# Performance work log

Hardware: AMD Instinct MI355X
Metric: run time of the kernel (lower is better)

Reference implementation:

```python
import jax, jax.numpy as jnp
import numpy as np
import math

G, NPG, D = 64, 2048, 128   # graphs, nodes per graph, feature dim
DEG = 16
N = G * NPG
E = N * DEG
VOCAB = 100000
RATIO = 0.8


def setup_inputs() -> dict:
    key = jax.random.key(0)
    ks = jax.random.split(key, 24)
    node_ids = jax.random.randint(ks[0], (N, 1), 0, VOCAB)
    # within-graph edges: endpoints in [0, NPG) per graph, then add graph offset
    within = jax.random.randint(ks[1], (2, G, NPG * DEG), 0, NPG)
    offs = (jnp.arange(G) * NPG)[None, :, None]
    edge_index = (within + offs).reshape(2, E)
    batch = jnp.repeat(jnp.arange(G), NPG)
    f = lambda k, shape: jax.random.normal(k, shape, dtype=jnp.float32) * 0.05
    return dict(
        node_ids=node_ids, edge_index=edge_index, batch=batch,
        emb=f(ks[2], (VOCAB, D)),
        Wl1=f(ks[3], (D, D)), Wr1=f(ks[4], (D, D)), bl1=f(ks[5], (D,)), pw1=f(ks[6], (D,)),
        Wl2=f(ks[7], (D, D)), Wr2=f(ks[8], (D, D)), bl2=f(ks[9], (D,)), pw2=f(ks[10], (D,)),
        Wl3=f(ks[11], (D, D)), Wr3=f(ks[12], (D, D)), bl3=f(ks[13], (D,)), pw3=f(ks[14], (D,)),
        W1=f(ks[15], (128, 256)), b1=f(ks[16], (128,)),
        W2=f(ks[17], (64, 128)), b2=f(ks[18], (64,)),
        W3=f(ks[19], (1, 64)), b3=f(ks[20], (1,)),
    )


def sage(x, src, dst, emask, Wl, bl, Wr):
    # PyG SAGEConv (mean aggr): lin_l(mean_j x_j) + lin_r(x_i); lin_r has no bias
    n = x.shape[0]
    msg = x[src] * emask[:, None].astype(x.dtype)
    dstm = jnp.where(emask, dst, n)  # dummy segment for invalid edges
    s = jax.ops.segment_sum(msg, dstm, num_segments=n + 1)[:n]
    c = jax.ops.segment_sum(emask.astype(x.dtype), dstm, num_segments=n + 1)[:n]
    mean = s / jnp.maximum(c, 1.0)[:, None]
    return mean @ Wl.T + bl + x @ Wr.T


def topk_pool(x, src, dst, emask, w, n_per):
    # PyG TopKPooling: score = tanh(x.w/||w||), keep top ceil(ratio*n) per graph,
    # scale kept features by score, remap/filter edges.
    n = x.shape[0]
    g = n // n_per
    k = math.ceil(RATIO * n_per)
    score = jnp.tanh((x @ w) / jnp.linalg.norm(w))
    ts, ti = jax.lax.top_k(score.reshape(g, n_per), k)  # [g, k]
    perm = (ti + (jnp.arange(g) * n_per)[:, None]).reshape(-1)  # old global idx
    x_new = x[perm] * ts.reshape(-1)[:, None]
    n_new = g * k
    new_of_old = jnp.full((n,), n_new, dtype=jnp.int32).at[perm].set(
        jnp.arange(n_new, dtype=jnp.int32))
    sn, dn = new_of_old[src], new_of_old[dst]
    em = emask & (sn < n_new) & (dn < n_new)
    sn = jnp.where(em, sn, 0)
    dn = jnp.where(em, dn, n_new)
    return x_new, sn, dn, em, k


def readout(x, k):
    # cat([global_max_pool, global_mean_pool]) with equal-size graphs
    g = x.shape[0] // k
    xr = x.reshape(g, k, -1)
    return jnp.concatenate([xr.max(axis=1), xr.mean(axis=1)], axis=1)


def reference(node_ids, edge_index, batch, emb,
              Wl1, Wr1, bl1, pw1, Wl2, Wr2, bl2, pw2, Wl3, Wr3, bl3, pw3,
              W1, b1, W2, b2, W3, b3):
    x = emb[node_ids.squeeze(1)]                       # [N, 128]
    src, dst = edge_index[0], edge_index[1]
    em = jnp.ones((src.shape[0],), dtype=bool)

    x = jax.nn.relu(sage(x, src, dst, em, Wl1, bl1, Wr1))
    x, src, dst, em, k1 = topk_pool(x, src, dst, em, pw1, NPG)
    x1 = readout(x, k1)

    x = jax.nn.relu(sage(x, src, dst, em, Wl2, bl2, Wr2))
    x, src, dst, em, k2 = topk_pool(x, src, dst, em, pw2, k1)
    x2 = readout(x, k2)

    x = jax.nn.relu(sage(x, src, dst, em, Wl3, bl3, Wr3))
    x, src, dst, em, k3 = topk_pool(x, src, dst, em, pw3, k2)
    x3 = readout(x, k3)

    h = x1 + x2 + x3                                   # [G, 256]
    h = jax.nn.relu(h @ W1.T + b1)
    h = jax.nn.relu(h @ W2.T + b2)                     # dropout = identity (eval)
    return jax.nn.sigmoid(h @ W3.T + b3).squeeze(1)    # [G]
```

## Files before the change

### kernel.cpp

```cpp
#include <hip/hip_runtime.h>
#include <hip/hip_bf16.h>
#include <float.h>

typedef _Float16 f16x8 __attribute__((ext_vector_type(8)));
typedef float f32x4 __attribute__((ext_vector_type(4)));

#define GRAPHS 64
#define NPG 2048
#define DIM 128
#define NNODES (GRAPHS * NPG)
#define NEDGES (NNODES * 16)
#define ECAP 32768
#define NSB 8
#define RSL 8
#define RPB 256

__global__ __launch_bounds__(256) void embed_kernel(const int* __restrict__ ids,
    const float* __restrict__ emb, _Float16* __restrict__ xh) {
  int idx = blockIdx.x * 256 + threadIdx.x;
  int nd = idx >> 4, part = idx & 15;
  int id = ids[nd];
  const float* src = emb + (size_t)id * 128 + part * 8;
  float4 a = *(const float4*)(src);
  float4 b = *(const float4*)(src + 4);
  f16x8 o;
  o[0] = (_Float16)a.x; o[1] = (_Float16)a.y; o[2] = (_Float16)a.z; o[3] = (_Float16)a.w;
  o[4] = (_Float16)b.x; o[5] = (_Float16)b.y; o[6] = (_Float16)b.z; o[7] = (_Float16)b.w;
  *(f16x8*)(xh + (size_t)nd * 128 + part * 8) = o;
}

__global__ __launch_bounds__(256) void convert_w(const float* __restrict__ Wl,
    const float* __restrict__ Wr, _Float16* __restrict__ wh) {
  int qq = blockIdx.x * 256 + threadIdx.x;
  int ks = qq >> 9, nf = (qq >> 6) & 7, l = qq & 63;
  int ncol = nf * 16 + (l & 15);
  int k0 = (ks & 3) * 32 + ((l >> 4) << 3);
  const float* wsrc = ((ks < 4) ? Wl : Wr) + ncol * 128 + k0;
  float4 a = *(const float4*)wsrc;
  float4 b = *(const float4*)(wsrc + 4);
  f16x8 w;
  w[0] = (_Float16)a.x; w[1] = (_Float16)a.y; w[2] = (_Float16)a.z; w[3] = (_Float16)a.w;
  w[4] = (_Float16)b.x; w[5] = (_Float16)b.y; w[6] = (_Float16)b.z; w[7] = (_Float16)b.w;
  *(f16x8*)(wh + (size_t)qq * 8) = w;
}

__global__ __launch_bounds__(1024) void csr_hist(const int* __restrict__ src,
    const int* __restrict__ dst, int np, int* __restrict__ part) {
  __shared__ int hist[2048];
  int x = blockIdx.x;
  int s = x & 7, q = x >> 3;
  int b = q & (NSB - 1), gh = q >> 3;
  int g = gh * 8 + s;
  int tid = threadIdx.x;
  for (int i = tid; i < 2048; i += 1024) hist[i] = 0;
  __syncthreads();
  int e0 = g * ECAP + b * (ECAP / NSB);
  int nodebase = g * np;
  for (int e = tid; e < ECAP / NSB; e += 1024) {
    atomicAdd(&hist[dst[e0 + e] - nodebase], 1);
  }
  __syncthreads();
  for (int i = tid; i < np; i += 1024) part[((size_t)(g * NSB + b)) * 2048 + i] = hist[i];
}

__global__ __launch_bounds__(1024) void csr_scan(const int* __restrict__ part, int np,
    int* __restrict__ offb, int* __restrict__ deg, int* __restrict__ curs) {
  __shared__ int psum[1024];
  int g = blockIdx.x, tid = threadIdx.x;
  int i0 = 2 * tid, i1 = 2 * tid + 1;
  int p0[NSB], p1[NSB];
  int c0 = 0, c1 = 0;
#pragma unroll
  for (int b = 0; b < NSB; ++b) {
    p0[b] = (i0 < np) ? part[((size_t)(g * NSB + b)) * 2048 + i0] : 0;
    p1[b] = (i1 < np) ? part[((size_t)(g * NSB + b)) * 2048 + i1] : 0;
    c0 += p0[b]; c1 += p1[b];
  }
  int pair = c0 + c1;
  psum[tid] = pair;
  for (int s = 1; s < 1024; s <<= 1) {
    __syncthreads();
    int t = (tid >= s) ? psum[tid - s] : 0;
    __syncthreads();
    psum[tid] += t;
  }
  int excl = psum[tid] - pair;
  int ebase = g * ECAP;
  int nodebase = g * np;
  if (i0 < np) {
    int off = ebase + excl;
    offb[nodebase + i0] = off;
    deg[nodebase + i0] = c0;
    int cur = off;
#pragma unroll
    for (int b = 0; b < NSB; ++b) { curs[((size_t)(g * NSB + b)) * 2048 + i0] = cur; cur += p0[b]; }
  }
  if (i1 < np) {
    int off = ebase + excl + c0;
    offb[nodebase + i1] = off;
    deg[nodebase + i1] = c1;
    int cur = off;
#pragma unroll
    for (int b = 0; b < NSB; ++b) { curs[((size_t)(g * NSB + b)) * 2048 + i1] = cur; cur += p1[b]; }
  }
}

__global__ __launch_bounds__(1024) void csr_place(const int* __restrict__ src,
    const int* __restrict__ dst, int np, const int* __restrict__ curs,
    int* __restrict__ esort) {
  __shared__ int cur[2048];
  int x = blockIdx.x;
  int s = x & 7, q = x >> 3;
  int b = q & (NSB - 1), gh = q >> 3;
  int g = gh * 8 + s;
  int tid = threadIdx.x;
  for (int i = tid; i < np; i += 1024) cur[i] = curs[((size_t)(g * NSB + b)) * 2048 + i];
  __syncthreads();
  int e0 = g * ECAP + b * (ECAP / NSB);
  int nodebase = g * np;
  for (int e = tid; e < ECAP / NSB; e += 1024) {
    int ge = e0 + e;
    int p = atomicAdd(&cur[dst[ge] - nodebase], 1);
    esort[p] = src[ge];
  }
}

__global__ __launch_bounds__(256) void remap_esort(const int* __restrict__ esort0,
    const int* __restrict__ noo, int* __restrict__ esortl, int E4) {
  int t = blockIdx.x * 256 + threadIdx.x;
  if (t >= E4) return;
  int4 s = *(const int4*)(esort0 + t * 4);
  int4 o;
  o.x = noo[s.x]; o.y = noo[s.y]; o.z = noo[s.z]; o.w = noo[s.w];
  *(int4*)(esortl + t * 4) = o;
}

__global__ __launch_bounds__(256) void aggregate_kernel(const _Float16* __restrict__ xh,
    const int* __restrict__ offb, const int* __restrict__ deg, const int* __restrict__ esrc,
    _Float16* __restrict__ meanh, int np, int C) {
  int bid = blockIdx.x;
  int s = bid & 7, q = bid >> 3;
  int gsub = q / C, chunk = q - gsub * C;
  int g = gsub * 8 + s;
  int wave = threadIdx.x >> 6, lane = threadIdx.x & 63;
  int sub = lane >> 4, l = lane & 15;
  int local = chunk * 16 + wave * 4 + sub;
  if (local >= np) return;
  int w = g * np + local;
  int b = offb[w], c = deg[w];
  int e = b + c;
  float acc[8] = {0.f, 0.f, 0.f, 0.f, 0.f, 0.f, 0.f, 0.f};
  int i = b;
  for (; i + 4 <= e; i += 4) {
    int s0 = esrc[i], s1 = esrc[i + 1], s2 = esrc[i + 2], s3 = esrc[i + 3];
    f16x8 v0 = *(const f16x8*)(xh + (size_t)s0 * 128 + l * 8);
    f16x8 v1 = *(const f16x8*)(xh + (size_t)s1 * 128 + l * 8);
    f16x8 v2 = *(const f16x8*)(xh + (size_t)s2 * 128 + l * 8);
    f16x8 v3 = *(const f16x8*)(xh + (size_t)s3 * 128 + l * 8);
    f16x8 t = (v0 + v1) + (v2 + v3);
#pragma unroll
    for (int j = 0; j < 8; ++j) acc[j] += (float)t[j];
  }
  for (; i < e; ++i) {
    int srcn = esrc[i];
    f16x8 v = *(const f16x8*)(xh + (size_t)srcn * 128 + l * 8);
#pragma unroll
    for (int j = 0; j < 8; ++j) acc[j] += (float)v[j];
  }
  float inv = 1.f / (float)(c > 0 ? c : 1);
  f16x8 o;
#pragma unroll
  for (int j = 0; j < 8; ++j) o[j] = (_Float16)(acc[j] * inv);
  *(f16x8*)(meanh + (size_t)w * 128 + l * 8) = o;
}

__global__ __launch_bounds__(256) void aggregate_f(const _Float16* __restrict__ xh,
    const int* __restrict__ offb0, const int* __restrict__ deg0, const int* __restrict__ esortl,
    const int* __restrict__ orig, _Float16* __restrict__ meanh, int np, int C) {
  int bid = blockIdx.x;
  int s = bid & 7, q = bid >> 3;
  int gsub = q / C, chunk = q - gsub * C;
  int g = gsub * 8 + s;
  int wave = threadIdx.x >> 6, lane = threadIdx.x & 63;
  int sub = lane >> 4, l = lane & 15;
  int local = chunk * 16 + wave * 4 + sub;
  if (local >= np) return;
  int w = g * np + local;
  int o = orig[w];
  int b = offb0[o], c0 = deg0[o];
  int e = b + c0;
  float acc[8] = {0.f, 0.f, 0.f, 0.f, 0.f, 0.f, 0.f, 0.f};
  int cnt = 0;
  const f16x8 zero = {(_Float16)0.f, (_Float16)0.f, (_Float16)0.f, (_Float16)0.f,
                      (_Float16)0.f, (_Float16)0.f, (_Float16)0.f, (_Float16)0.f};
  int i = b;
  for (; i + 4 <= e; i += 4) {
    int n0 = esortl[i], n1 = esortl[i + 1], n2 = esortl[i + 2], n3 = esortl[i + 3];
    f16x8 v0 = zero, v1 = zero, v2 = zero, v3 = zero;
    if (n0 >= 0) v0 = *(const f16x8*)(xh + (size_t)n0 * 128 + l * 8);
    if (n1 >= 0) v1 = *(const f16x8*)(xh + (size_t)n1 * 128 + l * 8);
    if (n2 >= 0) v2 = *(const f16x8*)(xh + (size_t)n2 * 128 + l * 8);
    if (n3 >= 0) v3 = *(const f16x8*)(xh + (size_t)n3 * 128 + l * 8);
    cnt += (n0 >= 0) + (n1 >= 0) + (n2 >= 0) + (n3 >= 0);
    f16x8 t = (v0 + v1) + (v2 + v3);
#pragma unroll
    for (int j = 0; j < 8; ++j) acc[j] += (float)t[j];
  }
  for (; i < e; ++i) {
    int sn = esortl[i];
    if (sn < 0) continue;
    ++cnt;
    f16x8 v = *(const f16x8*)(xh + (size_t)sn * 128 + l * 8);
#pragma unroll
    for (int j = 0; j < 8; ++j) acc[j] += (float)v[j];
  }
  float inv = 1.f / (float)(cnt > 0 ? cnt : 1);
  f16x8 ov;
#pragma unroll
  for (int j = 0; j < 8; ++j) ov[j] = (_Float16)(acc[j] * inv);
  *(f16x8*)(meanh + (size_t)w * 128 + l * 8) = ov;
}

__global__ __launch_bounds__(256, 2) void sage_gemm(const _Float16* __restrict__ XH,
    const _Float16* MEANIN, _Float16* OUT, const _Float16* __restrict__ WH,
    const float* __restrict__ bl, const float* __restrict__ pw, float* __restrict__ sc,
    int n) {
  __shared__ _Float16 WB[4096 * 8];
  int tid = threadIdx.x;
  for (int qq = tid; qq < 4096; qq += 256)
    *(f16x8*)(WB + qq * 8) = *(const f16x8*)(WH + (size_t)qq * 8);
  __syncthreads();
  int wave = tid >> 6, lane = tid & 63;
  int wrow0 = blockIdx.x * RPB + wave * 64;
  if (wrow0 >= n) return;
  int kb = (lane >> 4) << 3;
  int lr = lane & 15;
  f32x4 acc[4][8];
#pragma unroll
  for (int t = 0; t < 4; ++t)
#pragma unroll
    for (int nf = 0; nf < 8; ++nf) acc[t][nf] = (f32x4){0.f, 0.f, 0.f, 0.f};
#pragma unroll
  for (int ks = 0; ks < 8; ++ks) {
    const _Float16* A = (ks < 4) ? MEANIN : XH;
    const _Float16* ap = A + (size_t)(wrow0 + lr) * 128 + (ks & 3) * 32 + kb;
    f16x8 a0 = *(const f16x8*)(ap);
    f16x8 a1 = *(const f16x8*)(ap + 16 * 128);
    f16x8 a2 = *(const f16x8*)(ap + 32 * 128);
    f16x8 a3 = *(const f16x8*)(ap + 48 * 128);
#pragma unroll
    for (int nf = 0; nf < 8; ++nf) {
      f16x8 b = *(const f16x8*)(WB + ((ks * 8 + nf) * 64 + lane) * 8);
      acc[0][nf] = __builtin_amdgcn_mfma_f32_16x16x32_f16(a0, b, acc[0][nf], 0, 0, 0);
      acc[1][nf] = __builtin_amdgcn_mfma_f32_16x16x32_f16(a1, b, acc[1][nf], 0, 0, 0);
      acc[2][nf] = __builtin_amdgcn_mfma_f32_16x16x32_f16(a2, b, acc[2][nf], 0, 0, 0);
      acc[3][nf] = __builtin_amdgcn_mfma_f32_16x16x32_f16(a3, b, acc[3][nf], 0, 0, 0);
    }
  }
  float pwv[8], qn = 0.f;
#pragma unroll
  for (int nf = 0; nf < 8; ++nf) {
    pwv[nf] = pw[nf * 16 + lr];
    qn += pwv[nf] * pwv[nf];
  }
#pragma unroll
  for (int o = 1; o < 16; o <<= 1) qn += __shfl_xor(qn, o);
  float inv_n = 1.f / sqrtf(qn);
#pragma unroll
  for (int t = 0; t < 4; ++t) {
    int rbase = wrow0 + t * 16 + ((lane >> 4) << 2);
    float dot[4] = {0.f, 0.f, 0.f, 0.f};
#pragma unroll
    for (int nf = 0; nf < 8; ++nf) {
      int col = nf * 16 + lr;
      float bias = bl[col];
#pragma unroll
      for (int r = 0; r < 4; ++r) {
        float v = fmaxf(acc[t][nf][r] + bias, 0.f);
        OUT[(size_t)(rbase + r) * 128 + col] = (_Float16)v;
        dot[r] += v * pwv[nf];
      }
    }
#pragma unroll
    for (int r = 0; r < 4; ++r) {
#pragma unroll
      for (int o = 1; o < 16; o <<= 1) dot[r] += __shfl_xor(dot[r], o);
    }
    if (lr == 0) {
#pragma unroll
      for (int r = 0; r < 4; ++r) sc[rbase + r] = tanhf(dot[r] * inv_n);
    }
  }
}

__global__ __launch_bounds__(1024) void topk_sort(const float* __restrict__ sc,
    int n_per, int k, int* __restrict__ nooA, int* __restrict__ rankt, int mode) {
  __shared__ unsigned long long L[2048];
  __shared__ int c2n[2048];
  int g = blockIdx.x;
  int tid = threadIdx.x;
  int lane = tid & 63, wave = tid >> 6;
  int i0 = wave * 128 + lane;
  int i1 = i0 + 64;
  const float* scg = sc + g * n_per;
  auto keyize = [&](int i) -> unsigned long long {
    float f = (i < n_per) ? scg[i] : -FLT_MAX;
    unsigned u = __float_as_uint(f);
    u = (u & 0x80000000u) ? ~u : (u | 0x80000000u);
    return ((unsigned long long)u << 32) | (unsigned)(2047 - i);
  };
  unsigned long long a = keyize(i0), b = keyize(i1);
#pragma clang loop unroll(disable)
  for (unsigned kk = 2; kk <= 2048; kk <<= 1) {
#pragma clang loop unroll(disable)
    for (unsigned j = kk >> 1; j >= 128; j >>= 1) {
      L[i0] = a; L[i1] = b;
      __syncthreads();
      unsigned long long pa = L[i0 ^ j], pb = L[i1 ^ j];
      bool dA = ((i0 & kk) == 0), lA = ((i0 & j) == 0);
      if ((dA == lA) ? (pa > a) : (pa < a)) a = pa;
      bool dB = ((i1 & kk) == 0), lB = ((i1 & j) == 0);
      if ((dB == lB) ? (pb > b) : (pb < b)) b = pb;
      __syncthreads();
    }
    if (kk >= 128) {
      bool desc = ((i0 & kk) == 0);
      if ((a < b) == desc) { unsigned long long t = a; a = b; b = t; }
    }
    unsigned jtop = (kk >> 1 < 32u) ? (kk >> 1) : 32u;
#pragma clang loop unroll(disable)
    for (unsigned j = jtop; j >= 1; j >>= 1) {
      unsigned long long oa = __shfl_xor(a, (int)j);
      unsigned long long ob = __shfl_xor(b, (int)j);
      bool low = ((lane & j) == 0);
      bool dA = ((i0 & kk) == 0);
      if ((dA == low) ? (oa > a) : (oa < a)) a = oa;
      bool dB = ((i1 & kk) == 0);
      if ((dB == low) ? (ob > b) : (ob < b)) b = ob;
    }
  }
  int orig_a = 2047 - (int)(a & 0xFFFFFFFFu);
  int orig_b = 2047 - (int)(b & 0xFFFFFFFFu);
  if (i0 < k) rankt[g * NPG + i0] = orig_a;
  if (i1 < k) rankt[g * NPG + i1] = orig_b;
  if (mode == 0) {
    if (orig_a < n_per) nooA[g * n_per + orig_a] = (i0 < k) ? g * k + i0 : -1;
    if (orig_b < n_per) nooA[g * n_per + orig_b] = (i1 < k) ? g * k + i1 : -1;
  } else if (mode == 1) {
    if (orig_a < n_per) c2n[orig_a] = (i0 < k) ? g * k + i0 : -1;
    if (orig_b < n_per) c2n[orig_b] = (i1 < k) ? g * k + i1 : -1;
    __syncthreads();
    for (int o2 = tid; o2 < NPG; o2 += 1024) {
      int a0 = nooA[g * NPG + o2];
      nooA[g * NPG + o2] = (a0 >= 0) ? c2n[a0 - g * n_per] : -1;
    }
  }
}

__global__ __launch_bounds__(256) void topk_tail(const float* __restrict__ sc,
    const int* __restrict__ rankt, int n_per, int k, const _Float16* __restrict__ meanin,
    _Float16* __restrict__ xh, const int* __restrict__ orig_in, int* __restrict__ orig_out,
    float* __restrict__ pmax, float* __restrict__ psum) {
  int g = blockIdx.x >> 3;
  int slice = blockIdx.x & (RSL - 1);
  int rpb = (k + RSL - 1) / RSL;
  int r0 = slice * rpb;
  int r1 = r0 + rpb; if (r1 > k) r1 = k;
  const float* scg = sc + g * n_per;
  int grp = threadIdx.x >> 4, l8 = threadIdx.x & 15;
  float vmax[8], vsum[8];
#pragma unroll
  for (int j = 0; j < 8; ++j) { vmax[j] = -FLT_MAX; vsum[j] = 0.f; }
  for (int r = r0 + grp; r < r1; r += 16) {
    int orig = rankt[g * NPG + r];
    int p = g * n_per + orig;
    float score = scg[orig];
    f16x8 v = *(const f16x8*)(meanin + (size_t)p * 128 + l8 * 8);
    f16x8 ovv;
#pragma unroll
    for (int j = 0; j < 8; ++j) {
      float val = (float)v[j] * score;
      ovv[j] = (_Float16)val;
      vmax[j] = fmaxf(vmax[j], val);
      vsum[j] += val;
    }
    *(f16x8*)(xh + (size_t)(g * k + r) * 128 + l8 * 8) = ovv;
    if (l8 == 0) orig_out[g * k + r] = orig_in ? orig_in[p] : p;
  }
  __shared__ float smax[4 * 128], ssum[4 * 128];
  int lane = threadIdx.x & 63, wave = threadIdx.x >> 6;
#pragma unroll
  for (int j = 0; j < 8; ++j) {
    vmax[j] = fmaxf(vmax[j], __shfl_xor(vmax[j], 16));
    vmax[j] = fmaxf(vmax[j], __shfl_xor(vmax[j], 32));
    vsum[j] += __shfl_xor(vsum[j], 16);
    vsum[j] += __shfl_xor(vsum[j], 32);
  }
  if ((lane >> 4) == 0) {
#pragma unroll
    for (int j = 0; j < 8; ++j) {
      smax[wave * 128 + l8 * 8 + j] = vmax[j];
      ssum[wave * 128 + l8 * 8 + j] = vsum[j];
    }
  }
  __syncthreads();
  if (threadIdx.x < 128) {
    int d = threadIdx.x;
    float m = fmaxf(fmaxf(smax[d], smax[128 + d]), fmaxf(smax[256 + d], smax[384 + d]));
    float s2 = ssum[d] + ssum[128 + d] + ssum[256 + d] + ssum[384 + d];
    pmax[(size_t)(g * RSL + slice) * 128 + d] = m;
    psum[(size_t)(g * RSL + slice) * 128 + d] = s2;
  }
}

__global__ __launch_bounds__(256) void readout_comb(const float* __restrict__ pmax,
    const float* __restrict__ psum, int k, float* __restrict__ h) {
  int idx = blockIdx.x * 256 + threadIdx.x;
  int g = idx >> 7, d = idx & 127;
  float vmax = -FLT_MAX, vs = 0.f;
#pragma unroll
  for (int s = 0; s < RSL; ++s) {
    vmax = fmaxf(vmax, pmax[(size_t)(g * RSL + s) * 128 + d]);
    vs += psum[(size_t)(g * RSL + s) * 128 + d];
  }
  h[g * 256 + d] += vmax;
  h[g * 256 + 128 + d] += vs / (float)k;
}

__global__ __launch_bounds__(256) void mlp1(const float* __restrict__ h, const float* __restrict__ W1,
    const float* __restrict__ b1, float* __restrict__ h1) {
  int o = blockIdx.x * 256 + threadIdx.x;
  int g = o >> 7, j = o & 127;
  const float* hp = h + g * 256;
  const float* wp = W1 + j * 256;
  float a = b1[j];
  for (int c = 0; c < 256; ++c) a += hp[c] * wp[c];
  h1[o] = fmaxf(a, 0.f);
}

__global__ __launch_bounds__(256) void mlp2(const float* __restrict__ h1, const float* __restrict__ W2,
    const float* __restrict__ b2, float* __restrict__ h2) {
  int o = blockIdx.x * 256 + threadIdx.x;
  int g = o >> 6, j = o & 63;
  const float* hp = h1 + g * 128;
  const float* wp = W2 + j * 128;
  float a = b2[j];
  for (int c = 0; c < 128; ++c) a += hp[c] * wp[c];
  h2[o] = fmaxf(a, 0.f);
}

__global__ __launch_bounds__(64) void mlp3(const float* __restrict__ h2, const float* __restrict__ W3,
    const float* __restrict__ b3, float* __restrict__ out) {
  int g = threadIdx.x;
  if (g >= 64) return;
  const float* hp = h2 + g * 64;
  float a = b3[0];
  for (int c = 0; c < 64; ++c) a += hp[c] * W3[c];
  out[g] = 1.f / (1.f + expf(-a));
}

extern "C" void kernel_launch(void* const* d_in, const int* in_sizes, int n_in,
                              void* d_out, int out_size, void* d_ws, size_t ws_size,
                              hipStream_t stream) {
  const int* node_ids = (const int*)d_in[0];
  const int* ei = (const int*)d_in[1];
  const float* emb = (const float*)d_in[3];
  const float* W[3][4] = {
      {(const float*)d_in[4], (const float*)d_in[5], (const float*)d_in[6], (const float*)d_in[7]},
      {(const float*)d_in[8], (const float*)d_in[9], (const float*)d_in[10], (const float*)d_in[11]},
      {(const float*)d_in[12], (const float*)d_in[13], (const float*)d_in[14], (const float*)d_in[15]}};
  const float* W1 = (const float*)d_in[16];
  const float* b1 = (const float*)d_in[17];
  const float* W2 = (const float*)d_in[18];
  const float* b2 = (const float*)d_in[19];
  const float* W3 = (const float*)d_in[20];
  const float* b3 = (const float*)d_in[21];
  float* out = (float*)d_out;

  const int E = NEDGES;
  char* ws = (char*)d_ws;
  size_t o = 0;
  auto alloc = [&](size_t bytes) { void* p = ws + o; o = (o + bytes + 255) & ~(size_t)255; return p; };
  _Float16* XH = (_Float16*)alloc((size_t)NNODES * 128 * 2);
  _Float16* MEANH = (_Float16*)alloc((size_t)NNODES * 128 * 2);
  int* ESORT = (int*)alloc((size_t)E * 4);
  int* ESORTL = (int*)alloc((size_t)E * 4);
  int* PART = (int*)alloc((size_t)GRAPHS * NSB * 2048 * 4);
  int* CURS = (int*)alloc((size_t)GRAPHS * NSB * 2048 * 4);
  int* OFFB = (int*)alloc((size_t)NNODES * 4);
  int* DEG = (int*)alloc((size_t)NNODES * 4);
  float* SC = (float*)alloc((size_t)NNODES * 4);
  int* NOOA = (int*)alloc((size_t)NNODES * 4);
  int* RANKT = (int*)alloc((size_t)NNODES * 4);
  int* ORIGA = (int*)alloc((size_t)NNODES * 4);
  int* ORIGB = (int*)alloc((size_t)NNODES * 4);
  _Float16* WH0 = (_Float16*)alloc(4096 * 8 * 2);
  _Float16* WH1 = (_Float16*)alloc(4096 * 8 * 2);
  _Float16* WH2 = (_Float16*)alloc(4096 * 8 * 2);
  float* PMAX = (float*)alloc((size_t)GRAPHS * RSL * 128 * 4);
  float* PSUM = (float*)alloc((size_t)GRAPHS * RSL * 128 * 4);
  float* H = (float*)alloc(64 * 256 * 4);
  float* H1 = (float*)alloc(64 * 128 * 4);
  float* H2 = (float*)alloc(64 * 64 * 4);

  embed_kernel<<<NNODES * 16 / 256, 256, 0, stream>>>(node_ids, emb, XH);
  hipMemsetAsync(H, 0, 64 * 256 * 4, stream);
  convert_w<<<16, 256, 0, stream>>>(W[0][0], W[0][1], WH0);
  convert_w<<<16, 256, 0, stream>>>(W[1][0], W[1][1], WH1);
  convert_w<<<16, 256, 0, stream>>>(W[2][0], W[2][1], WH2);

  const int* src = ei;
  const int* dst = ei + E;
  csr_hist<<<GRAPHS * NSB, 1024, 0, stream>>>(src, dst, NPG, PART);
  csr_scan<<<GRAPHS, 1024, 0, stream>>>(PART, NPG, OFFB, DEG, CURS);
  csr_place<<<GRAPHS * NSB, 1024, 0, stream>>>(src, dst, NPG, CURS, ESORT);

  struct LayerP { int n, k; };
  LayerP L[3] = {{131072, 1639}, {104896, 1312}, {83968, 1050}};
  _Float16* WHs[3] = {WH0, WH1, WH2};
  int* ORIG_cur = ORIGA;
  int* ORIG_next = ORIGB;

  for (int li = 0; li < 3; ++li) {
    int n = L[li].n, k = L[li].k;
    int np = n / 64;
    const float *bl = W[li][2], *pw = W[li][3];

    int C = (np + 15) / 16;
    if (li == 0) {
      aggregate_kernel<<<64 * C, 256, 0, stream>>>(XH, OFFB, DEG, ESORT, MEANH, np, C);
    } else {
      remap_esort<<<E / 4 / 256, 256, 0, stream>>>(ESORT, NOOA, ESORTL, E / 4);
      aggregate_f<<<64 * C, 256, 0, stream>>>(XH, OFFB, DEG, ESORTL, ORIG_cur,
                                              MEANH, np, C);
    }
    sage_gemm<<<(n + RPB - 1) / RPB, 256, 0, stream>>>(XH, MEANH, MEANH, WHs[li], bl, pw, SC, n);
    topk_sort<<<GRAPHS, 1024, 0, stream>>>(SC, np, k, NOOA, RANKT, li);
    topk_tail<<<GRAPHS * RSL, 256, 0, stream>>>(SC, RANKT, np, k, MEANH, XH,
        (li == 0) ? nullptr : ORIG_cur, ORIG_next, PMAX, PSUM);
    readout_comb<<<32, 256, 0, stream>>>(PMAX, PSUM, k, H);
    { int* t = ORIG_cur; ORIG_cur = ORIG_next; ORIG_next = t; }
  }

  mlp1<<<32, 256, 0, stream>>>(H, W1, b1, H1);
  mlp2<<<16, 256, 0, stream>>>(H1, W2, b2, H2);
  mlp3<<<1, 64, 0, stream>>>(H2, W3, b3, out);
}
```

Baseline: 363.4 us.

## Fuse readout combine and MLP head, merge weight conversions, double readout slices

Merges the three weight-conversion launches into one kernel and removes the memset of the head accumulator. The per-layer readout_comb kernel and the three MLP kernels are replaced by a single per-graph kernel that reduces all three layers' partial max/sum buffers and runs the MLP in shared memory. The number of topk_tail slices per graph is doubled to spread the readout work across more blocks. This cuts about nine small kernel launches, at the cost of larger partial buffers and a head kernel that launches only 64 blocks.

```diff
diff --git a/kernel.cpp b/kernel.cpp
--- a/kernel.cpp
+++ b/kernel.cpp
@@ -12,7 +12,7 @@
 #define NEDGES (NNODES * 16)
 #define ECAP 32768
 #define NSB 8
-#define RSL 8
+#define RSL 16
 #define RPB 256
 
 __global__ __launch_bounds__(256) void embed_kernel(const int* __restrict__ ids,
@@ -29,9 +29,15 @@
   *(f16x8*)(xh + (size_t)nd * 128 + part * 8) = o;
 }
 
-__global__ __launch_bounds__(256) void convert_w(const float* __restrict__ Wl,
-    const float* __restrict__ Wr, _Float16* __restrict__ wh) {
-  int qq = blockIdx.x * 256 + threadIdx.x;
+__global__ __launch_bounds__(256) void convert_w3(const float* __restrict__ Wl0,
+    const float* __restrict__ Wr0, const float* __restrict__ Wl1, const float* __restrict__ Wr1,
+    const float* __restrict__ Wl2, const float* __restrict__ Wr2,
+    _Float16* __restrict__ wh0, _Float16* __restrict__ wh1, _Float16* __restrict__ wh2) {
+  int li = blockIdx.x >> 4;
+  int qq = (blockIdx.x & 15) * 256 + threadIdx.x;
+  const float* Wl = (li == 0) ? Wl0 : ((li == 1) ? Wl1 : Wl2);
+  const float* Wr = (li == 0) ? Wr0 : ((li == 1) ? Wr1 : Wr2);
+  _Float16* wh = (li == 0) ? wh0 : ((li == 1) ? wh1 : wh2);
   int ks = qq >> 9, nf = (qq >> 6) & 7, l = qq & 63;
   int ncol = nf * 16 + (l & 15);
   int k0 = (ks & 3) * 32 + ((l >> 4) << 3);
@@ -361,7 +367,7 @@
     const int* __restrict__ rankt, int n_per, int k, const _Float16* __restrict__ meanin,
     _Float16* __restrict__ xh, const int* __restrict__ orig_in, int* __restrict__ orig_out,
     float* __restrict__ pmax, float* __restrict__ psum) {
-  int g = blockIdx.x >> 3;
+  int g = blockIdx.x >> 4;
   int slice = blockIdx.x & (RSL - 1);
   int rpb = (k + RSL - 1) / RSL;
   int r0 = slice * rpb;
@@ -413,50 +419,53 @@
   }
 }
 
-__global__ __launch_bounds__(256) void readout_comb(const float* __restrict__ pmax,
-    const float* __restrict__ psum, int k, float* __restrict__ h) {
-  int idx = blockIdx.x * 256 + threadIdx.x;
-  int g = idx >> 7, d = idx & 127;
-  float vmax = -FLT_MAX, vs = 0.f;
-#pragma unroll
-  for (int s = 0; s < RSL; ++s) {
-    vmax = fmaxf(vmax, pmax[(size_t)(g * RSL + s) * 128 + d]);
-    vs += psum[(size_t)(g * RSL + s) * 128 + d];
-  }
-  h[g * 256 + d] += vmax;
-  h[g * 256 + 128 + d] += vs / (float)k;
-}
-
-__global__ __launch_bounds__(256) void mlp1(const float* __restrict__ h, const float* __restrict__ W1,
-    const float* __restrict__ b1, float* __restrict__ h1) {
-  int o = blockIdx.x * 256 + threadIdx.x;
-  int g = o >> 7, j = o & 127;
-  const float* hp = h + g * 256;
-  const float* wp = W1 + j * 256;
-  float a = b1[j];
-  for (int c = 0; c < 256; ++c) a += hp[c] * wp[c];
-  h1[o] = fmaxf(a, 0.f);
-}
-
-__global__ __launch_bounds__(256) void mlp2(const float* __restrict__ h1, const float* __restrict__ W2,
-    const float* __restrict__ b2, float* __restrict__ h2) {
-  int o = blockIdx.x * 256 + threadIdx.x;
-  int g = o >> 6, j = o & 63;
-  const float* hp = h1 + g * 128;
-  const float* wp = W2 + j * 128;
-  float a = b2[j];
-  for (int c = 0; c < 128; ++c) a += hp[c] * wp[c];
-  h2[o] = fmaxf(a, 0.f);
-}
-
-__global__ __launch_bounds__(64) void mlp3(const float* __restrict__ h2, const float* __restrict__ W3,
-    const float* __restrict__ b3, float* __restrict__ out) {
-  int g = threadIdx.x;
-  if (g >= 64) return;
-  const float* hp = h2 + g * 64;
-  float a = b3[0];
-  for (int c = 0; c < 64; ++c) a += hp[c] * W3[c];
-  out[g] = 1.f / (1.f + expf(-a));
+__global__ __launch_bounds__(256) void mlp_fused(const float* __restrict__ pmax,
+    const float* __restrict__ psum, int k0, int k1, int k2,
+    const float* __restrict__ W1, const float* __restrict__ b1,
+    const float* __restrict__ W2, const float* __restrict__ b2,
+    const float* __restrict__ W3, const float* __restrict__ b3, float* __restrict__ out) {
+  __shared__ float h[256], h1[128], h2[64];
+  int g = blockIdx.x, t = threadIdx.x;
+  int ks[3] = {k0, k1, k2};
+  if (t < 128) {
+    float hm = 0.f, hs = 0.f;
+#pragma unroll
+    for (int li = 0; li < 3; ++li) {
+      const float* pm = pmax + ((size_t)li * GRAPHS + g) * RSL * 128;
+      const float* ps = psum + ((size_t)li * GRAPHS + g) * RSL * 128;
+      float m = -FLT_MAX, s = 0.f;
+#pragma unroll
+      for (int sl = 0; sl < RSL; ++sl) {
+        m = fmaxf(m, pm[sl * 128 + t]);
+        s += ps[sl * 128 + t];
+      }
+      hm += m;
+      hs += s / (float)ks[li];
+    }
+    h[t] = hm;
+    h[128 + t] = hs;
+  }
+  __syncthreads();
+  if (t < 128) {
+    const float* wp = W1 + t * 256;
+    float a = b1[t];
+    for (int c = 0; c < 256; ++c) a += h[c] * wp[c];
+    h1[t] = fmaxf(a, 0.f);
+  }
+  __syncthreads();
+  if (t < 64) {
+    const float* wp = W2 + t * 128;
+    float a = b2[t];
+    for (int c = 0; c < 128; ++c) a += h1[c] * wp[c];
+    h2[t] = fmaxf(a, 0.f);
+  }
+  __syncthreads();
+  if (t < 64) {
+    float a = h2[t] * W3[t];
+#pragma unroll
+    for (int o = 32; o >= 1; o >>= 1) a += __shfl_xor(a, o);
+    if (t == 0) out[g] = 1.f / (1.f + expf(-(a + b3[0])));
+  }
 }
 
 extern "C" void kernel_launch(void* const* d_in, const int* in_sizes, int n_in,
@@ -497,17 +506,12 @@
   _Float16* WH0 = (_Float16*)alloc(4096 * 8 * 2);
   _Float16* WH1 = (_Float16*)alloc(4096 * 8 * 2);
   _Float16* WH2 = (_Float16*)alloc(4096 * 8 * 2);
-  float* PMAX = (float*)alloc((size_t)GRAPHS * RSL * 128 * 4);
-  float* PSUM = (float*)alloc((size_t)GRAPHS * RSL * 128 * 4);
-  float* H = (float*)alloc(64 * 256 * 4);
-  float* H1 = (float*)alloc(64 * 128 * 4);
-  float* H2 = (float*)alloc(64 * 64 * 4);
+  float* PMAX = (float*)alloc((size_t)3 * GRAPHS * RSL * 128 * 4);
+  float* PSUM = (float*)alloc((size_t)3 * GRAPHS * RSL * 128 * 4);
 
   embed_kernel<<<NNODES * 16 / 256, 256, 0, stream>>>(node_ids, emb, XH);
-  hipMemsetAsync(H, 0, 64 * 256 * 4, stream);
-  convert_w<<<16, 256, 0, stream>>>(W[0][0], W[0][1], WH0);
-  convert_w<<<16, 256, 0, stream>>>(W[1][0], W[1][1], WH1);
-  convert_w<<<16, 256, 0, stream>>>(W[2][0], W[2][1], WH2);
+  convert_w3<<<48, 256, 0, stream>>>(W[0][0], W[0][1], W[1][0], W[1][1], W[2][0], W[2][1],
+                                     WH0, WH1, WH2);
 
   const int* src = ei;
   const int* dst = ei + E;
@@ -537,12 +541,11 @@
     sage_gemm<<<(n + RPB - 1) / RPB, 256, 0, stream>>>(XH, MEANH, MEANH, WHs[li], bl, pw, SC, n);
     topk_sort<<<GRAPHS, 1024, 0, stream>>>(SC, np, k, NOOA, RANKT, li);
     topk_tail<<<GRAPHS * RSL, 256, 0, stream>>>(SC, RANKT, np, k, MEANH, XH,
-        (li == 0) ? nullptr : ORIG_cur, ORIG_next, PMAX, PSUM);
-    readout_comb<<<32, 256, 0, stream>>>(PMAX, PSUM, k, H);
+        (li == 0) ? nullptr : ORIG_cur, ORIG_next,
+        PMAX + (size_t)li * GRAPHS * RSL * 128, PSUM + (size_t)li * GRAPHS * RSL * 128);
     { int* t = ORIG_cur; ORIG_cur = ORIG_next; ORIG_next = t; }
   }
 
-  mlp1<<<32, 256, 0, stream>>>(H, W1, b1, H1);
-  mlp2<<<16, 256, 0, stream>>>(H1, W2, b2, H2);
-  mlp3<<<1, 64, 0, stream>>>(H2, W3, b3, out);
-}
+  mlp_fused<<<GRAPHS, 256, 0, stream>>>(PMAX, PSUM, L[0].k, L[1].k, L[2].k,
+                                        W1, b1, W2, b2, W3, b3, out);
+}
```

Measured after the change: 331.6 us. 8.7% less time.
